# Performance work log

Hardware: AMD Instinct MI355X
Metric: run time of the kernel (lower is better)

The kernel has to match this reference:

```python
import jax, jax.numpy as jnp
import numpy as np

B, C, H, W, R = 8, 256, 64, 64, 16


def setup_inputs() -> dict:
    key = jax.random.key(0)
    ks = jax.random.split(key, 14)
    def w(k, shape, fan):
        return (jax.random.normal(k, shape, jnp.float32) / np.sqrt(fan)).astype(jnp.float32)
    return {
        "features_depth": jax.random.normal(ks[0], (B, C, H, W), jnp.float32),
        "features_semseg": jax.random.normal(ks[1], (B, C, H, W), jnp.float32),
        "W0": w(ks[2], (C, 2 * C), 2 * C),          # conv_split0 1x1, [out,in]
        "Wdw": w(ks[3], (C, 1, 3, 3), 9),            # depthwise 3x3, groups=C
        "Wq": w(ks[4], (C, C), C),                   # Linear weights [out,in]
        "Wk": w(ks[5], (C, C), C),
        "Wv": w(ks[6], (C, C), C),
        "Wp": w(ks[7], (C, C), C),
        "bp": jnp.zeros((C,), jnp.float32),
        "Wsplit": w(ks[8], (C, C), C),               # conv_split 1x1
        "se_d_w1": w(ks[9], (C // R, C), C),         # SE squeeze conv1x1 (depth)
        "se_d_w2": w(ks[10], (C, C // R), C // R),
        "se_s_w1": w(ks[11], (C // R, C), C),        # SE squeeze conv1x1 (semseg)
        "se_s_w2": w(ks[12], (C, C // R), C // R),
    }


def _l2norm(a, eps=1e-12):
    n = jnp.linalg.norm(a, axis=-1, keepdims=True)
    return a / jnp.maximum(n, eps)


def _se(x, w1, w2):
    # x: [B,C,H,W]; global avg pool -> 1x1 convs -> sigmoid gate
    p = x.mean(axis=(2, 3))                                  # [B,C]
    h = jax.nn.relu(jnp.einsum('rc,bc->br', w1, p))          # [B,C/R]
    g = jax.nn.sigmoid(jnp.einsum('cr,br->bc', w2, h))       # [B,C]
    return x * g[:, :, None, None]


def reference(features_depth, features_semseg, W0, Wdw, Wq, Wk, Wv, Wp, bp,
              Wsplit, se_d_w1, se_d_w2, se_s_w1, se_s_w2):
    x = jnp.concatenate([features_depth, features_semseg], axis=1)  # [B,2C,H,W]
    x = jnp.einsum('oc,bchw->bohw', W0, x)                          # 1x1 conv
    x = jax.lax.conv_general_dilated(
        x, Wdw, window_strides=(1, 1), padding='SAME',
        dimension_numbers=('NCHW', 'OIHW', 'NCHW'), feature_group_count=C)
    xt = x.transpose(0, 2, 3, 1).reshape(B, H * W, C)               # [B,N,C]
    q = (xt @ Wq.T).transpose(0, 2, 1)                              # [B,C,N]
    k = (xt @ Wk.T).transpose(0, 2, 1)
    v = (xt @ Wv.T).transpose(0, 2, 1)
    q = _l2norm(q)
    k = _l2norm(k)
    attn = jax.nn.softmax(jnp.einsum('bcn,bdn->bcd', k, q), axis=-1)  # [B,C,C]
    y = jnp.einsum('bcd,bdn->bcn', attn, v)                         # [B,C,N]
    y = y.transpose(0, 2, 1)                                        # [B,N,C]
    y = y @ Wp.T + bp                                               # proj
    out_c = y.reshape(B, H, W, C).transpose(0, 3, 1, 2)             # [B,C,H,W]
    out_c = jnp.einsum('oc,bchw->bohw', Wsplit, out_c)              # 1x1 conv
    out_depth = _se(out_c, se_d_w1, se_d_w2) + features_depth
    out_semseg = _se(out_c, se_s_w1, se_s_w2) + features_semseg
    return (out_depth, out_semseg)
```

## Files before the change

kernel.cpp:

```cpp
#include <hip/hip_runtime.h>
#include <cstdint>

#define DEVI __device__ __forceinline__

using fx4 = __attribute__((ext_vector_type(4))) float;
using bf8 = __attribute__((ext_vector_type(8))) __bf16;
using s8v = __attribute__((ext_vector_type(8))) short;
using s4v = __attribute__((ext_vector_type(4))) short;
typedef unsigned short u16;
typedef unsigned int u32;

DEVI float b2f(u16 u) { return __builtin_bit_cast(float, (u32)u << 16); }
DEVI u16 f2b(float f) {
  u32 u = __builtin_bit_cast(u32, f);
  return (u16)((u + 0x7fffu + ((u >> 16) & 1u)) >> 16);
}

#define GLOAD(g, l)                                                          \
  __builtin_amdgcn_global_load_lds(                                          \
      (const __attribute__((address_space(1))) unsigned int*)(g),            \
      (__attribute__((address_space(3))) unsigned int*)(l), 16, 0, 0)

__global__ __launch_bounds__(256) void prep(const float* __restrict__ W0,
                                            const float* __restrict__ Wq,
                                            const float* __restrict__ Wk,
                                            const float* __restrict__ Wv,
                                            u16* __restrict__ w0b,
                                            u16* __restrict__ wqk2,
                                            u16* __restrict__ wvtb) {
  const int i = blockIdx.x * 256 + threadIdx.x;
  if (blockIdx.y == 0) {
    if (i < 131072) w0b[i] = f2b(W0[i]);
  } else if (blockIdx.y == 1) {
    if (i < 524288) {
      const int row = i >> 9, c = i & 511;
      const float* src = (row < 256) ? Wq : Wk;
      wqk2[i] = f2b(src[((row & 255) << 8) + (c & 255)]);
    }
  } else {
    if (i < 65536) {
      const int e = i >> 8, d = i & 255;
      wvtb[i] = f2b(Wv[d * 256 + e]);
    }
  }
}

__global__ __launch_bounds__(256) void wcmul(const float* __restrict__ Wsp,
                                             const float* __restrict__ Wp,
                                             const float* __restrict__ bp,
                                             u16* __restrict__ wcb, float* __restrict__ bc) {
  const int o = blockIdx.x, t = threadIdx.x;
  __shared__ float row[256];
  __shared__ float red[4];
  row[t] = Wsp[o * 256 + t];
  __syncthreads();
  float acc = 0.f;
  for (int c = 0; c < 256; ++c) acc += row[c] * Wp[c * 256 + t];
  wcb[o * 256 + t] = f2b(acc);
  float pb = row[t] * bp[t];
#pragma unroll
  for (int m = 32; m > 0; m >>= 1) pb += __shfl_xor(pb, m);
  if ((t & 63) == 0) red[t >> 6] = pb;
  __syncthreads();
  if (t == 0) bc[o] = red[0] + red[1] + red[2] + red[3];
}

__global__ void pack_cat(const float* __restrict__ fd, const float* __restrict__ fs,
                         u16* __restrict__ out) {
  __shared__ float t[32][33];
  const int b = blockIdx.z;
  const int n0 = blockIdx.x * 32;
  const int g = blockIdx.y;
  const float* src = (g < 8) ? fd : fs;
  const int c0 = (g & 7) * 32;
  const int ccol0 = g * 32;
  const int tx = threadIdx.x;
  const int ty = threadIdx.y;
  const float* sp = src + ((long)b * 256 + c0) * 4096 + n0;
#pragma unroll
  for (int i = 0; i < 4; ++i) {
    int c = ty + i * 8;
    t[c][tx] = sp[(long)c * 4096 + tx];
  }
  __syncthreads();
  u16* op = out + ((long)b * 4096 + n0) * 512 + ccol0;
#pragma unroll
  for (int i = 0; i < 4; ++i) {
    int r = ty + i * 8;
    op[(long)r * 512 + tx] = f2b(t[tx][r]);
  }
}

template <typename OT, int BIAS, bool POOL>
__global__ __launch_bounds__(256) void gemm_nt(
    const u16* __restrict__ A, long sA, int lda,
    const u16* __restrict__ B, long sB, int ldb,
    OT* __restrict__ C, long sC, long sCs, int ldc,
    const float* __restrict__ bias, int Keff, int ksplit,
    float* __restrict__ poolpart) {
  __shared__ u16 ldsA[128 * 64];
  __shared__ u16 ldsB[128 * 64];
  const int z = blockIdx.z;
  const int bb = z / ksplit;
  const int ss = z - bb * ksplit;
  const int bm = blockIdx.x * 128;
  const int bn = blockIdx.y * 128;
  const u16* Ab = A + bb * sA + (long)ss * Keff + (long)bm * lda;
  const u16* Bb = B + bb * sB + (long)ss * Keff + (long)bn * ldb;
  const int tid = threadIdx.x;
  const int wid = tid >> 6;
  const int lane = tid & 63;
  const int wm = wid >> 1, wn = wid & 1;
  const int srow = tid >> 3;
  const int slot = tid & 7;

  fx4 acc[4][4] = {};
  for (int kt = 0; kt < Keff; kt += 64) {
#pragma unroll
    for (int i = 0; i < 4; ++i) {
      const int row = i * 32 + srow;
      const int kq = slot ^ (row & 7);
      GLOAD(Ab + (long)row * lda + kt + kq * 8, &ldsA[i * 2048 + wid * 512]);
      GLOAD(Bb + (long)row * ldb + kt + kq * 8, &ldsB[i * 2048 + wid * 512]);
    }
    __syncthreads();
#pragma unroll
    for (int ko = 0; ko < 2; ++ko) {
      bf8 af[4], bfr[4];
      const int kq = ko * 4 + (lane >> 4);
#pragma unroll
      for (int f = 0; f < 4; ++f) {
        const int ar = wm * 64 + f * 16 + (lane & 15);
        af[f] = *(const bf8*)&ldsA[ar * 64 + ((kq ^ (ar & 7)) * 8)];
        const int br = wn * 64 + f * 16 + (lane & 15);
        bfr[f] = *(const bf8*)&ldsB[br * 64 + ((kq ^ (br & 7)) * 8)];
      }
#pragma unroll
      for (int fm = 0; fm < 4; ++fm)
#pragma unroll
        for (int fn = 0; fn < 4; ++fn)
          acc[fm][fn] = __builtin_amdgcn_mfma_f32_16x16x32_bf16(af[fm], bfr[fn], acc[fm][fn], 0, 0, 0);
    }
    __syncthreads();
  }
  OT* Cb = C + bb * sC + ss * sCs;
  float pr[4][4];
  if (POOL) {
#pragma unroll
    for (int fm = 0; fm < 4; ++fm)
#pragma unroll
      for (int r = 0; r < 4; ++r) pr[fm][r] = 0.f;
  }
#pragma unroll
  for (int fm = 0; fm < 4; ++fm) {
    const int m0 = bm + wm * 64 + fm * 16 + ((lane >> 4) << 2);
#pragma unroll
    for (int fn = 0; fn < 4; ++fn) {
      const int n0 = bn + wn * 64 + fn * 16 + (lane & 15);
#pragma unroll
      for (int r = 0; r < 4; ++r) {
        float v = acc[fm][fn][r];
        if (BIAS == 2) v += bias[m0 + r];
        if constexpr (sizeof(OT) == 2) Cb[(long)(m0 + r) * ldc + n0] = (OT)f2b(v);
        else Cb[(long)(m0 + r) * ldc + n0] = v;
        if (POOL) pr[fm][r] += v;
      }
    }
  }
  if (POOL) {
#pragma unroll
    for (int fm = 0; fm < 4; ++fm)
#pragma unroll
      for (int r = 0; r < 4; ++r) {
        float s = pr[fm][r];
        s += __shfl_xor(s, 1); s += __shfl_xor(s, 2);
        s += __shfl_xor(s, 4); s += __shfl_xor(s, 8);
        if ((lane & 15) == 0) {
          const int o = bm + wm * 64 + fm * 16 + ((lane >> 4) << 2) + r;
          poolpart[(long)(blockIdx.y * 2 + wn) * 2048 + bb * 256 + o] = s;
        }
      }
  }
}

__global__ __launch_bounds__(256) void dwconv3x3(const u16* __restrict__ x,
                                                 const float* __restrict__ wdw,
                                                 u16* __restrict__ y) {
  __shared__ float w[9][256];
  const int t = threadIdx.x;
  for (int i = t; i < 2304; i += 256) w[i % 9][i / 9] = wdw[i];
  __syncthreads();
  const int nb = blockIdx.x;
  const int b = nb >> 9;
  const int n0 = (nb & 511) << 3;
  const int tn = t >> 5;
  const int tc = (t & 31) << 3;
  const int n = n0 + tn;
  const int hh = n >> 6, ww2 = n & 63;
  const u16* base = x + ((long)b << 20);
  float acc[8] = {0.f, 0.f, 0.f, 0.f, 0.f, 0.f, 0.f, 0.f};
#pragma unroll
  for (int ky = 0; ky < 3; ++ky) {
    const int hy = hh + ky - 1;
    if ((unsigned)hy >= 64u) continue;
#pragma unroll
    for (int kx = 0; kx < 3; ++kx) {
      const int wx = ww2 + kx - 1;
      if ((unsigned)wx >= 64u) continue;
      const s8v v = *(const s8v*)&base[(((hy << 6) + wx) << 8) + tc];
      const int kk = ky * 3 + kx;
      const fx4 wa = *(const fx4*)&w[kk][tc];
      const fx4 wb = *(const fx4*)&w[kk][tc + 4];
#pragma unroll
      for (int j = 0; j < 4; ++j) {
        acc[j] += wa[j] * b2f((u16)v[j]);
        acc[4 + j] += wb[j] * b2f((u16)v[4 + j]);
      }
    }
  }
  s8v o;
#pragma unroll
  for (int j = 0; j < 8; ++j) o[j] = (short)f2b(acc[j]);
  *(s8v*)&y[((long)b << 20) + ((long)n << 8) + tc] = o;
}

__global__ void btrans(const u16* __restrict__ x, u16* __restrict__ y) {
  __shared__ u16 t[32][34];
  const int b = blockIdx.z;
  const int n0 = blockIdx.x * 32;
  const int c0 = blockIdx.y * 32;
  const int tx = threadIdx.x, ty = threadIdx.y;
  const u16* sp = x + (long)b * 1048576 + (long)n0 * 256 + c0;
#pragma unroll
  for (int j = 0; j < 4; ++j) {
    int i = ty + j * 8;
    t[i][tx] = sp[(long)i * 256 + tx];
  }
  __syncthreads();
  u16* op = y + (long)b * 1048576 + (long)c0 * 4096 + n0;
#pragma unroll
  for (int j = 0; j < 4; ++j) {
    int r = ty + j * 8;
    op[(long)r * 4096 + tx] = t[tx][r];
  }
}

__global__ __launch_bounds__(256) void gsplit(const float* __restrict__ part,
                                              u16* __restrict__ G2) {
  const int i4 = (blockIdx.x * 256 + threadIdx.x) * 4;
  fx4 s = {0.f, 0.f, 0.f, 0.f};
#pragma unroll
  for (int ss = 0; ss < 8; ++ss) s += *(const fx4*)(part + (long)ss * 524288 + i4);
  const int b = i4 >> 16, rem = i4 & 65535, e = rem >> 8, c0 = rem & 255;
  u16* d = G2 + (long)b * 131072 + (long)e * 512 + c0;
  s4v hi, lo;
#pragma unroll
  for (int j = 0; j < 4; ++j) {
    u16 h = f2b(s[j]);
    hi[j] = (short)h;
    lo[j] = (short)f2b(s[j] - b2f(h));
  }
  *(s4v*)d = hi;
  *(s4v*)(d + 256) = lo;
}

__global__ __launch_bounds__(256) void ssplit_diag(const float* __restrict__ SS,
                                                   const float* __restrict__ Wq,
                                                   const float* __restrict__ Wk,
                                                   u16* __restrict__ S2,
                                                   float* __restrict__ rinv) {
  const int wid = threadIdx.x >> 6, lane = threadIdx.x & 63;
  const int gid = blockIdx.x * 4 + wid;
  const int b = gid >> 9, row = gid & 511;
  const float* ssrow = SS + (long)b * 131072 + (long)row * 256;
  const float* wrow = (row < 256) ? (Wq + row * 256) : (Wk + (row - 256) * 256);
  const fx4 sv = ((const fx4*)ssrow)[lane];
  const fx4 wv = ((const fx4*)wrow)[lane];
  float dot = sv[0] * wv[0] + sv[1] * wv[1] + sv[2] * wv[2] + sv[3] * wv[3];
#pragma unroll
  for (int o = 32; o > 0; o >>= 1) dot += __shfl_xor(dot, o);
  if (lane == 0)
    rinv[b * 512 + row] = 1.f / fmaxf(sqrtf(fmaxf(dot, 0.f)), 1e-12f);
  if (row < 256) {
    u16* d = S2 + (long)b * 131072 + (long)row * 512 + lane * 4;
    s4v hi, lo;
#pragma unroll
    for (int j = 0; j < 4; ++j) {
      u16 h = f2b(sv[j]);
      hi[j] = (short)h;
      lo[j] = (short)f2b(sv[j] - b2f(h));
    }
    *(s4v*)d = hi;
    *(s4v*)(d + 256) = lo;
  }
}

__global__ __launch_bounds__(256) void softmax_g(const float* __restrict__ araw,
                                                 const float* __restrict__ rinv,
                                                 u16* __restrict__ out) {
  const int wid = threadIdx.x >> 6, lane = threadIdx.x & 63;
  const long row = (long)blockIdx.x * 4 + wid;
  const int b = (int)(row >> 8);
  const int c = (int)(row & 255);
  fx4 v = ((const fx4*)(araw + row * 256))[lane];
  const float rk = rinv[b * 512 + 256 + c];
  const fx4 rq = *(const fx4*)&rinv[b * 512 + lane * 4];
  v[0] *= rk * rq[0]; v[1] *= rk * rq[1]; v[2] *= rk * rq[2]; v[3] *= rk * rq[3];
  float m = fmaxf(fmaxf(v[0], v[1]), fmaxf(v[2], v[3]));
#pragma unroll
  for (int o = 32; o > 0; o >>= 1) m = fmaxf(m, __shfl_xor(m, o));
  float e0 = __expf(v[0] - m), e1 = __expf(v[1] - m);
  float e2 = __expf(v[2] - m), e3 = __expf(v[3] - m);
  float s4 = e0 + e1 + e2 + e3;
#pragma unroll
  for (int o = 32; o > 0; o >>= 1) s4 += __shfl_xor(s4, o);
  const float inv = 1.f / s4;
  u16* op = out + row * 256 + lane * 4;
  op[0] = f2b(e0 * inv); op[1] = f2b(e1 * inv);
  op[2] = f2b(e2 * inv); op[3] = f2b(e3 * inv);
}

__global__ __launch_bounds__(256) void se_gates(const float* __restrict__ poolpart,
                                                const float* __restrict__ w1d, const float* __restrict__ w2d,
                                                const float* __restrict__ w1s, const float* __restrict__ w2s,
                                                float* __restrict__ gd, float* __restrict__ gs) {
  const int b = blockIdx.x;
  const int t = threadIdx.x;
  __shared__ float p[256], hd[16], hs[16];
  float s = 0.f;
#pragma unroll 8
  for (int sl = 0; sl < 64; ++sl) s += poolpart[(long)sl * 2048 + b * 256 + t];
  p[t] = s * (1.f / 4096.f);
  __syncthreads();
  if (t < 16) {
    float ad = 0.f, as2 = 0.f;
    for (int j = 0; j < 256; ++j) {
      ad += w1d[t * 256 + j] * p[j];
      as2 += w1s[t * 256 + j] * p[j];
    }
    hd[t] = fmaxf(ad, 0.f);
    hs[t] = fmaxf(as2, 0.f);
  }
  __syncthreads();
  float ad = 0.f, as2 = 0.f;
#pragma unroll
  for (int r = 0; r < 16; ++r) {
    ad += w2d[t * 16 + r] * hd[r];
    as2 += w2s[t * 16 + r] * hs[r];
  }
  gd[b * 256 + t] = 1.f / (1.f + __expf(-ad));
  gs[b * 256 + t] = 1.f / (1.f + __expf(-as2));
}

__global__ __launch_bounds__(256) void fuse_out(const u16* __restrict__ oc,
                                                const float* __restrict__ gd, const float* __restrict__ gs,
                                                const float* __restrict__ fd, const float* __restrict__ fs,
                                                float* __restrict__ od, float* __restrict__ os) {
  const long i = ((long)blockIdx.x * 256 + threadIdx.x) * 8;
  const long bc = i >> 12;
  const float gdv = gd[bc], gsv = gs[bc];
  const s8v c8 = *(const s8v*)&oc[i];
  const fx4 a0 = *(const fx4*)(fd + i), a1 = *(const fx4*)(fd + i + 4);
  const fx4 s0 = *(const fx4*)(fs + i), s1 = *(const fx4*)(fs + i + 4);
  fx4 d0, d1, e0, e1;
#pragma unroll
  for (int j = 0; j < 4; ++j) {
    const float cl = b2f((u16)c8[j]);
    const float ch = b2f((u16)c8[4 + j]);
    d0[j] = cl * gdv + a0[j]; d1[j] = ch * gdv + a1[j];
    e0[j] = cl * gsv + s0[j]; e1[j] = ch * gsv + s1[j];
  }
  *(fx4*)(od + i) = d0; *(fx4*)(od + i + 4) = d1;
  *(fx4*)(os + i) = e0; *(fx4*)(os + i + 4) = e1;
}

extern "C" void kernel_launch(void* const* d_in, const int* in_sizes, int n_in,
                              void* d_out, int out_size, void* d_ws, size_t ws_size,
                              hipStream_t stream) {
  const float* fd  = (const float*)d_in[0];
  const float* fs  = (const float*)d_in[1];
  const float* W0  = (const float*)d_in[2];
  const float* Wdw = (const float*)d_in[3];
  const float* Wq  = (const float*)d_in[4];
  const float* Wk  = (const float*)d_in[5];
  const float* Wv  = (const float*)d_in[6];
  const float* Wp  = (const float*)d_in[7];
  const float* bp  = (const float*)d_in[8];
  const float* Wsp = (const float*)d_in[9];
  const float* w1d = (const float*)d_in[10];
  const float* w2d = (const float*)d_in[11];
  const float* w1s = (const float*)d_in[12];
  const float* w2s = (const float*)d_in[13];

  char* ws = (char*)d_ws;
  u16* catb   = (u16*)(ws + 0);
  u16* xtT    = (u16*)(ws + 0);
  u16* x0b    = (u16*)(ws + 33554432);
  u16* outcb  = x0b;
  u16* xtb    = (u16*)(ws + 50331648);
  float* part = (float*)(ws + 67108864);
  u16* G2     = (u16*)(ws + 83886080);
  float* SS   = (float*)(ws + 85983232);
  u16* S2     = (u16*)(ws + 90177536);
  float* araw = (float*)(ws + 92274688);
  u16* attnb  = (u16*)(ws + 94371840);
  u16* m1t    = (u16*)(ws + 95420416);
  u16* wfin   = (u16*)(ws + 96468992);
  u16* w0b    = (u16*)(ws + 97517568);
  u16* wqk2   = (u16*)(ws + 97779712);
  u16* wvtb   = (u16*)(ws + 98304000);
  u16* wcb    = (u16*)(ws + 98435072);
  float* bcb  = (float*)(ws + 98566144);
  float* rinv = (float*)(ws + 98567168);
  float* poolpart = (float*)(ws + 98583552);
  float* gdp  = (float*)(ws + 99108864);
  float* gsp  = (float*)(ws + 99117056);
  float* od  = (float*)d_out;
  float* osg = od + 8388608;

  prep<<<dim3(2048, 3), 256, 0, stream>>>(W0, Wq, Wk, Wv, w0b, wqk2, wvtb);
  wcmul<<<256, 256, 0, stream>>>(Wsp, Wp, bp, wcb, bcb);
  pack_cat<<<dim3(128, 16, 8), dim3(32, 8), 0, stream>>>(fd, fs, catb);
  gemm_nt<u16, 0, false><<<dim3(32, 2, 8), 256, 0, stream>>>(
      catb, 2097152, 512, w0b, 0, 512, x0b, 1048576, 0, 256, nullptr, 512, 1, nullptr);
  dwconv3x3<<<4096, 256, 0, stream>>>(x0b, Wdw, xtb);
  btrans<<<dim3(128, 8, 8), dim3(32, 8), 0, stream>>>(xtb, xtT);
  gemm_nt<float, 0, false><<<dim3(2, 2, 64), 256, 0, stream>>>(
      xtT, 1048576, 4096, xtT, 1048576, 4096,
      part, 65536, 524288, 256, nullptr, 512, 8, nullptr);
  gsplit<<<512, 256, 0, stream>>>(part, G2);
  gemm_nt<float, 0, false><<<dim3(4, 2, 8), 256, 0, stream>>>(
      wqk2, 0, 512, G2, 131072, 512, SS, 131072, 0, 256, nullptr, 512, 1, nullptr);
  ssplit_diag<<<1024, 256, 0, stream>>>(SS, Wq, Wk, S2, rinv);
  gemm_nt<float, 0, false><<<dim3(2, 2, 8), 256, 0, stream>>>(
      wqk2 + 131072, 0, 512, S2, 131072, 512, araw, 65536, 0, 256, nullptr, 512, 1, nullptr);
  softmax_g<<<512, 256, 0, stream>>>(araw, rinv, attnb);
  gemm_nt<u16, 0, false><<<dim3(2, 2, 8), 256, 0, stream>>>(
      wvtb, 0, 256, attnb, 65536, 256, m1t, 65536, 0, 256, nullptr, 256, 1, nullptr);
  gemm_nt<u16, 0, false><<<dim3(2, 2, 8), 256, 0, stream>>>(
      wcb, 0, 256, m1t, 65536, 256, wfin, 65536, 0, 256, nullptr, 256, 1, nullptr);
  gemm_nt<u16, 2, true><<<dim3(2, 32, 8), 256, 0, stream>>>(
      wfin, 65536, 256, xtb, 1048576, 256, outcb, 1048576, 0, 4096, bcb, 256, 1, poolpart);
  se_gates<<<8, 256, 0, stream>>>(poolpart, w1d, w2d, w1s, w2s, gdp, gsp);
  fuse_out<<<4096, 256, 0, stream>>>(outcb, gdp, gsp, fd, fs, od, osg);
}
```

Baseline: 183.9 us.

## Fuse dwconv with transpose, fold ssplit into GEMM epilogue, residual from bf16 cat

The depthwise conv now also writes the channel-major transposed copy through LDS, which removes the separate btrans kernel. The Gram GEMM uses a deeper K per split with fewer splits, so gsplit sums 4 partials instead of 8. The SS GEMM epilogue writes the hi/lo bf16 split directly and computes the partial diagonal norms, which removes ssplit_diag and its fp32 SS buffer. Softmax now reduces those partials itself. The final fuse reads the residual from the bf16 packed concat instead of the fp32 inputs, which cuts traffic but rounds the residual add to bf16 precision.

```diff
diff --git a/kernel.cpp b/kernel.cpp
--- a/kernel.cpp
+++ b/kernel.cpp
@@ -91,13 +91,15 @@
   }
 }
 
-template <typename OT, int BIAS, bool POOL>
+template <typename OT, int BIAS, bool POOL, int EPI>
 __global__ __launch_bounds__(256) void gemm_nt(
     const u16* __restrict__ A, long sA, int lda,
     const u16* __restrict__ B, long sB, int ldb,
     OT* __restrict__ C, long sC, long sCs, int ldc,
     const float* __restrict__ bias, int Keff, int ksplit,
-    float* __restrict__ poolpart) {
+    float* __restrict__ poolpart,
+    const float* __restrict__ wqf, const float* __restrict__ wkf,
+    float* __restrict__ dpart) {
   __shared__ u16 ldsA[128 * 64];
   __shared__ u16 ldsB[128 * 64];
   const int z = blockIdx.z;
@@ -143,6 +145,47 @@
     }
     __syncthreads();
   }
+  if constexpr (EPI == 1) {
+    u16* S2b = (u16*)C + bb * sC;
+    float dp[4][4];
+#pragma unroll
+    for (int fm = 0; fm < 4; ++fm)
+#pragma unroll
+      for (int r = 0; r < 4; ++r) dp[fm][r] = 0.f;
+#pragma unroll
+    for (int fm = 0; fm < 4; ++fm) {
+      const int m0 = bm + wm * 64 + fm * 16 + ((lane >> 4) << 2);
+#pragma unroll
+      for (int fn = 0; fn < 4; ++fn) {
+        const int n0 = bn + wn * 64 + fn * 16 + (lane & 15);
+#pragma unroll
+        for (int r = 0; r < 4; ++r) {
+          const float v = acc[fm][fn][r];
+          const int m = m0 + r;
+          if (m < 256) {
+            const u16 hi = f2b(v);
+            S2b[(long)m * 512 + n0] = hi;
+            S2b[(long)m * 512 + 256 + n0] = f2b(v - b2f(hi));
+          }
+          const float* wr = (m < 256) ? (wqf + (long)m * 256) : (wkf + (long)(m - 256) * 256);
+          dp[fm][r] += v * wr[n0];
+        }
+      }
+    }
+#pragma unroll
+    for (int fm = 0; fm < 4; ++fm)
+#pragma unroll
+      for (int r = 0; r < 4; ++r) {
+        float s = dp[fm][r];
+        s += __shfl_xor(s, 1); s += __shfl_xor(s, 2);
+        s += __shfl_xor(s, 4); s += __shfl_xor(s, 8);
+        if ((lane & 15) == 0) {
+          const int m = bm + wm * 64 + fm * 16 + ((lane >> 4) << 2) + r;
+          dpart[(long)(blockIdx.y * 2 + wn) * 4096 + bb * 512 + m] = s;
+        }
+      }
+    return;
+  }
   OT* Cb = C + bb * sC + ss * sCs;
   float pr[4][4];
   if (POOL) {
@@ -183,66 +226,53 @@
   }
 }
 
-__global__ __launch_bounds__(256) void dwconv3x3(const u16* __restrict__ x,
-                                                 const float* __restrict__ wdw,
-                                                 u16* __restrict__ y) {
-  __shared__ float w[9][256];
+__global__ __launch_bounds__(256) void dwconv2(const u16* __restrict__ x,
+                                               const float* __restrict__ wdw,
+                                               u16* __restrict__ y,
+                                               u16* __restrict__ yT) {
+  __shared__ float wsm[9][256];
+  __shared__ u16 tb[256][72];
   const int t = threadIdx.x;
-  for (int i = t; i < 2304; i += 256) w[i % 9][i / 9] = wdw[i];
-  __syncthreads();
-  const int nb = blockIdx.x;
-  const int b = nb >> 9;
-  const int n0 = (nb & 511) << 3;
-  const int tn = t >> 5;
-  const int tc = (t & 31) << 3;
-  const int n = n0 + tn;
-  const int hh = n >> 6, ww2 = n & 63;
+  for (int i = t; i < 2304; i += 256) wsm[i % 9][i / 9] = wdw[i];
+  const int b = blockIdx.x >> 6, h = blockIdx.x & 63;
+  const int c8 = (t & 31) * 8, wsub = t >> 5;
   const u16* base = x + ((long)b << 20);
-  float acc[8] = {0.f, 0.f, 0.f, 0.f, 0.f, 0.f, 0.f, 0.f};
-#pragma unroll
-  for (int ky = 0; ky < 3; ++ky) {
-    const int hy = hh + ky - 1;
-    if ((unsigned)hy >= 64u) continue;
-#pragma unroll
-    for (int kx = 0; kx < 3; ++kx) {
-      const int wx = ww2 + kx - 1;
-      if ((unsigned)wx >= 64u) continue;
-      const s8v v = *(const s8v*)&base[(((hy << 6) + wx) << 8) + tc];
-      const int kk = ky * 3 + kx;
-      const fx4 wa = *(const fx4*)&w[kk][tc];
-      const fx4 wb = *(const fx4*)&w[kk][tc + 4];
-#pragma unroll
-      for (int j = 0; j < 4; ++j) {
-        acc[j] += wa[j] * b2f((u16)v[j]);
-        acc[4 + j] += wb[j] * b2f((u16)v[4 + j]);
-      }
-    }
-  }
-  s8v o;
-#pragma unroll
-  for (int j = 0; j < 8; ++j) o[j] = (short)f2b(acc[j]);
-  *(s8v*)&y[((long)b << 20) + ((long)n << 8) + tc] = o;
-}
-
-__global__ void btrans(const u16* __restrict__ x, u16* __restrict__ y) {
-  __shared__ u16 t[32][34];
-  const int b = blockIdx.z;
-  const int n0 = blockIdx.x * 32;
-  const int c0 = blockIdx.y * 32;
-  const int tx = threadIdx.x, ty = threadIdx.y;
-  const u16* sp = x + (long)b * 1048576 + (long)n0 * 256 + c0;
-#pragma unroll
-  for (int j = 0; j < 4; ++j) {
-    int i = ty + j * 8;
-    t[i][tx] = sp[(long)i * 256 + tx];
-  }
-  __syncthreads();
-  u16* op = y + (long)b * 1048576 + (long)c0 * 4096 + n0;
-#pragma unroll
-  for (int j = 0; j < 4; ++j) {
-    int r = ty + j * 8;
-    op[(long)r * 4096 + tx] = t[tx][r];
-  }
+  __syncthreads();
+#pragma unroll
+  for (int i = 0; i < 8; ++i) {
+    const int w = wsub + 8 * i;
+    float acc[8] = {0.f, 0.f, 0.f, 0.f, 0.f, 0.f, 0.f, 0.f};
+#pragma unroll
+    for (int ky = 0; ky < 3; ++ky) {
+      const int hy = h + ky - 1;
+      if ((unsigned)hy >= 64u) continue;
+#pragma unroll
+      for (int kx = 0; kx < 3; ++kx) {
+        const int wx = w + kx - 1;
+        if ((unsigned)wx >= 64u) continue;
+        const s8v v = *(const s8v*)&base[(((hy << 6) + wx) << 8) + c8];
+        const int kk = ky * 3 + kx;
+        const fx4 wa = *(const fx4*)&wsm[kk][c8];
+        const fx4 wb = *(const fx4*)&wsm[kk][c8 + 4];
+#pragma unroll
+        for (int j = 0; j < 4; ++j) {
+          acc[j] += wa[j] * b2f((u16)v[j]);
+          acc[4 + j] += wb[j] * b2f((u16)v[4 + j]);
+        }
+      }
+    }
+    s8v o;
+#pragma unroll
+    for (int j = 0; j < 8; ++j) o[j] = (short)f2b(acc[j]);
+    *(s8v*)&y[((long)b << 20) + (long)(((h << 6) + w) << 8) + c8] = o;
+#pragma unroll
+    for (int j = 0; j < 8; ++j) tb[c8 + j][w] = (u16)o[j];
+  }
+  __syncthreads();
+  u16* dst = yT + ((long)b << 20) + (long)t * 4096 + (h << 6);
+#pragma unroll
+  for (int j = 0; j < 8; ++j)
+    *(s8v*)&dst[j * 8] = *(const s8v*)&tb[t][j * 8];
 }
 
 __global__ __launch_bounds__(256) void gsplit(const float* __restrict__ part,
@@ -250,7 +280,7 @@
   const int i4 = (blockIdx.x * 256 + threadIdx.x) * 4;
   fx4 s = {0.f, 0.f, 0.f, 0.f};
 #pragma unroll
-  for (int ss = 0; ss < 8; ++ss) s += *(const fx4*)(part + (long)ss * 524288 + i4);
+  for (int ss = 0; ss < 4; ++ss) s += *(const fx4*)(part + (long)ss * 524288 + i4);
   const int b = i4 >> 16, rem = i4 & 65535, e = rem >> 8, c0 = rem & 255;
   u16* d = G2 + (long)b * 131072 + (long)e * 512 + c0;
   s4v hi, lo;
@@ -264,48 +294,25 @@
   *(s4v*)(d + 256) = lo;
 }
 
-__global__ __launch_bounds__(256) void ssplit_diag(const float* __restrict__ SS,
-                                                   const float* __restrict__ Wq,
-                                                   const float* __restrict__ Wk,
-                                                   u16* __restrict__ S2,
-                                                   float* __restrict__ rinv) {
+__global__ __launch_bounds__(256) void softmax_g2(const float* __restrict__ araw,
+                                                  const float* __restrict__ dpart,
+                                                  u16* __restrict__ out) {
   const int wid = threadIdx.x >> 6, lane = threadIdx.x & 63;
-  const int gid = blockIdx.x * 4 + wid;
-  const int b = gid >> 9, row = gid & 511;
-  const float* ssrow = SS + (long)b * 131072 + (long)row * 256;
-  const float* wrow = (row < 256) ? (Wq + row * 256) : (Wk + (row - 256) * 256);
-  const fx4 sv = ((const fx4*)ssrow)[lane];
-  const fx4 wv = ((const fx4*)wrow)[lane];
-  float dot = sv[0] * wv[0] + sv[1] * wv[1] + sv[2] * wv[2] + sv[3] * wv[3];
-#pragma unroll
-  for (int o = 32; o > 0; o >>= 1) dot += __shfl_xor(dot, o);
-  if (lane == 0)
-    rinv[b * 512 + row] = 1.f / fmaxf(sqrtf(fmaxf(dot, 0.f)), 1e-12f);
-  if (row < 256) {
-    u16* d = S2 + (long)b * 131072 + (long)row * 512 + lane * 4;
-    s4v hi, lo;
-#pragma unroll
-    for (int j = 0; j < 4; ++j) {
-      u16 h = f2b(sv[j]);
-      hi[j] = (short)h;
-      lo[j] = (short)f2b(sv[j] - b2f(h));
-    }
-    *(s4v*)d = hi;
-    *(s4v*)(d + 256) = lo;
-  }
-}
-
-__global__ __launch_bounds__(256) void softmax_g(const float* __restrict__ araw,
-                                                 const float* __restrict__ rinv,
-                                                 u16* __restrict__ out) {
-  const int wid = threadIdx.x >> 6, lane = threadIdx.x & 63;
+  const int t = threadIdx.x;
+  const int b = blockIdx.x >> 6;
+  __shared__ float rq[256];
+  float dq = dpart[b * 512 + t] + dpart[4096 + b * 512 + t] +
+             dpart[8192 + b * 512 + t] + dpart[12288 + b * 512 + t];
+  rq[t] = 1.f / fmaxf(sqrtf(fmaxf(dq, 0.f)), 1e-12f);
+  __syncthreads();
   const long row = (long)blockIdx.x * 4 + wid;
-  const int b = (int)(row >> 8);
   const int c = (int)(row & 255);
+  const int ki = b * 512 + 256 + c;
+  float dk = dpart[ki] + dpart[4096 + ki] + dpart[8192 + ki] + dpart[12288 + ki];
+  const float rk = 1.f / fmaxf(sqrtf(fmaxf(dk, 0.f)), 1e-12f);
   fx4 v = ((const fx4*)(araw + row * 256))[lane];
-  const float rk = rinv[b * 512 + 256 + c];
-  const fx4 rq = *(const fx4*)&rinv[b * 512 + lane * 4];
-  v[0] *= rk * rq[0]; v[1] *= rk * rq[1]; v[2] *= rk * rq[2]; v[3] *= rk * rq[3];
+  v[0] *= rk * rq[lane * 4];     v[1] *= rk * rq[lane * 4 + 1];
+  v[2] *= rk * rq[lane * 4 + 2]; v[3] *= rk * rq[lane * 4 + 3];
   float m = fmaxf(fmaxf(v[0], v[1]), fmaxf(v[2], v[3]));
 #pragma unroll
   for (int o = 32; o > 0; o >>= 1) m = fmaxf(m, __shfl_xor(m, o));
@@ -352,26 +359,47 @@
   gs[b * 256 + t] = 1.f / (1.f + __expf(-as2));
 }
 
-__global__ __launch_bounds__(256) void fuse_out(const u16* __restrict__ oc,
-                                                const float* __restrict__ gd, const float* __restrict__ gs,
-                                                const float* __restrict__ fd, const float* __restrict__ fs,
-                                                float* __restrict__ od, float* __restrict__ os) {
-  const long i = ((long)blockIdx.x * 256 + threadIdx.x) * 8;
-  const long bc = i >> 12;
-  const float gdv = gd[bc], gsv = gs[bc];
-  const s8v c8 = *(const s8v*)&oc[i];
-  const fx4 a0 = *(const fx4*)(fd + i), a1 = *(const fx4*)(fd + i + 4);
-  const fx4 s0 = *(const fx4*)(fs + i), s1 = *(const fx4*)(fs + i + 4);
-  fx4 d0, d1, e0, e1;
+__global__ __launch_bounds__(256) void fuse_out2(const u16* __restrict__ oc,
+                                                 const u16* __restrict__ cat,
+                                                 const float* __restrict__ gd,
+                                                 const float* __restrict__ gs,
+                                                 float* __restrict__ od,
+                                                 float* __restrict__ os) {
+  __shared__ u16 td[32][68];
+  __shared__ u16 ts2[32][68];
+  const int b = blockIdx.z;
+  const int c0 = blockIdx.y * 32;
+  const int n0 = blockIdx.x * 64;
+  const int t = threadIdx.x;
+  {
+    const int n = t >> 2, cj = (t & 3) * 8;
+    const u16* cb = cat + ((long)b * 4096 + n0 + n) * 512 + c0 + cj;
+    const s8v vd = *(const s8v*)cb;
+    const s8v vs = *(const s8v*)(cb + 256);
+#pragma unroll
+    for (int j = 0; j < 8; ++j) {
+      td[cj + j][n] = (u16)vd[j];
+      ts2[cj + j][n] = (u16)vs[j];
+    }
+  }
+  __syncthreads();
+  const int c = t >> 3, no = (t & 7) * 8;
+  const long obase = ((long)b * 256 + c0 + c) * 4096 + n0 + no;
+  const float gdv = gd[b * 256 + c0 + c];
+  const float gsv = gs[b * 256 + c0 + c];
+  const s8v o8 = *(const s8v*)&oc[obase];
+  fx4 r0, r1, q0, q1;
 #pragma unroll
   for (int j = 0; j < 4; ++j) {
-    const float cl = b2f((u16)c8[j]);
-    const float ch = b2f((u16)c8[4 + j]);
-    d0[j] = cl * gdv + a0[j]; d1[j] = ch * gdv + a1[j];
-    e0[j] = cl * gsv + s0[j]; e1[j] = ch * gsv + s1[j];
-  }
-  *(fx4*)(od + i) = d0; *(fx4*)(od + i + 4) = d1;
-  *(fx4*)(os + i) = e0; *(fx4*)(os + i + 4) = e1;
+    const float vl = b2f((u16)o8[j]);
+    const float vh = b2f((u16)o8[4 + j]);
+    r0[j] = vl * gdv + b2f(td[c][no + j]);
+    r1[j] = vh * gdv + b2f(td[c][no + 4 + j]);
+    q0[j] = vl * gsv + b2f(ts2[c][no + j]);
+    q1[j] = vh * gsv + b2f(ts2[c][no + 4 + j]);
+  }
+  *(fx4*)(od + obase) = r0; *(fx4*)(od + obase + 4) = r1;
+  *(fx4*)(os + obase) = q0; *(fx4*)(os + obase + 4) = q1;
 }
 
 extern "C" void kernel_launch(void* const* d_in, const int* in_sizes, int n_in,
@@ -394,53 +422,56 @@
 
   char* ws = (char*)d_ws;
   u16* catb   = (u16*)(ws + 0);
-  u16* xtT    = (u16*)(ws + 0);
   u16* x0b    = (u16*)(ws + 33554432);
   u16* outcb  = x0b;
   u16* xtb    = (u16*)(ws + 50331648);
-  float* part = (float*)(ws + 67108864);
-  u16* G2     = (u16*)(ws + 83886080);
-  float* SS   = (float*)(ws + 85983232);
-  u16* S2     = (u16*)(ws + 90177536);
-  float* araw = (float*)(ws + 92274688);
-  u16* attnb  = (u16*)(ws + 94371840);
-  u16* m1t    = (u16*)(ws + 95420416);
-  u16* wfin   = (u16*)(ws + 96468992);
-  u16* w0b    = (u16*)(ws + 97517568);
-  u16* wqk2   = (u16*)(ws + 97779712);
-  u16* wvtb   = (u16*)(ws + 98304000);
-  u16* wcb    = (u16*)(ws + 98435072);
-  float* bcb  = (float*)(ws + 98566144);
-  float* rinv = (float*)(ws + 98567168);
-  float* poolpart = (float*)(ws + 98583552);
-  float* gdp  = (float*)(ws + 99108864);
-  float* gsp  = (float*)(ws + 99117056);
+  u16* xtT    = (u16*)(ws + 67108864);
+  float* part = (float*)(ws + 83886080);
+  u16* G2     = (u16*)(ws + 92274688);
+  u16* S2     = (u16*)(ws + 94371840);
+  float* araw = (float*)(ws + 96468992);
+  u16* attnb  = (u16*)(ws + 98566144);
+  u16* m1t    = (u16*)(ws + 99614720);
+  u16* wfin   = (u16*)(ws + 100663296);
+  u16* w0b    = (u16*)(ws + 101711872);
+  u16* wqk2   = (u16*)(ws + 101974016);
+  u16* wvtb   = (u16*)(ws + 102498304);
+  u16* wcb    = (u16*)(ws + 102629376);
+  float* bcb  = (float*)(ws + 102760448);
+  float* dpart = (float*)(ws + 102761472);
+  float* poolpart = (float*)(ws + 102827008);
+  float* gdp  = (float*)(ws + 103351296);
+  float* gsp  = (float*)(ws + 103359488);
   float* od  = (float*)d_out;
   float* osg = od + 8388608;
 
   prep<<<dim3(2048, 3), 256, 0, stream>>>(W0, Wq, Wk, Wv, w0b, wqk2, wvtb);
   wcmul<<<256, 256, 0, stream>>>(Wsp, Wp, bp, wcb, bcb);
   pack_cat<<<dim3(128, 16, 8), dim3(32, 8), 0, stream>>>(fd, fs, catb);
-  gemm_nt<u16, 0, false><<<dim3(32, 2, 8), 256, 0, stream>>>(
-      catb, 2097152, 512, w0b, 0, 512, x0b, 1048576, 0, 256, nullptr, 512, 1, nullptr);
-  dwconv3x3<<<4096, 256, 0, stream>>>(x0b, Wdw, xtb);
-  btrans<<<dim3(128, 8, 8), dim3(32, 8), 0, stream>>>(xtb, xtT);
-  gemm_nt<float, 0, false><<<dim3(2, 2, 64), 256, 0, stream>>>(
+  gemm_nt<u16, 0, false, 0><<<dim3(32, 2, 8), 256, 0, stream>>>(
+      catb, 2097152, 512, w0b, 0, 512, x0b, 1048576, 0, 256, nullptr, 512, 1,
+      nullptr, nullptr, nullptr, nullptr);
+  dwconv2<<<512, 256, 0, stream>>>(x0b, Wdw, xtb, xtT);
+  gemm_nt<float, 0, false, 0><<<dim3(2, 2, 32), 256, 0, stream>>>(
       xtT, 1048576, 4096, xtT, 1048576, 4096,
-      part, 65536, 524288, 256, nullptr, 512, 8, nullptr);
+      part, 65536, 524288, 256, nullptr, 1024, 4, nullptr, nullptr, nullptr, nullptr);
   gsplit<<<512, 256, 0, stream>>>(part, G2);
-  gemm_nt<float, 0, false><<<dim3(4, 2, 8), 256, 0, stream>>>(
-      wqk2, 0, 512, G2, 131072, 512, SS, 131072, 0, 256, nullptr, 512, 1, nullptr);
-  ssplit_diag<<<1024, 256, 0, stream>>>(SS, Wq, Wk, S2, rinv);
-  gemm_nt<float, 0, false><<<dim3(2, 2, 8), 256, 0, stream>>>(
-      wqk2 + 131072, 0, 512, S2, 131072, 512, araw, 65536, 0, 256, nullptr, 512, 1, nullptr);
-  softmax_g<<<512, 256, 0, stream>>>(araw, rinv, attnb);
-  gemm_nt<u16, 0, false><<<dim3(2, 2, 8), 256, 0, stream>>>(
-      wvtb, 0, 256, attnb, 65536, 256, m1t, 65536, 0, 256, nullptr, 256, 1, nullptr);
-  gemm_nt<u16, 0, false><<<dim3(2, 2, 8), 256, 0, stream>>>(
-      wcb, 0, 256, m1t, 65536, 256, wfin, 65536, 0, 256, nullptr, 256, 1, nullptr);
-  gemm_nt<u16, 2, true><<<dim3(2, 32, 8), 256, 0, stream>>>(
-      wfin, 65536, 256, xtb, 1048576, 256, outcb, 1048576, 0, 4096, bcb, 256, 1, poolpart);
+  gemm_nt<u16, 0, false, 1><<<dim3(4, 2, 8), 256, 0, stream>>>(
+      wqk2, 0, 512, G2, 131072, 512, S2, 131072, 0, 512, nullptr, 512, 1,
+      nullptr, Wq, Wk, dpart);
+  gemm_nt<float, 0, false, 0><<<dim3(2, 2, 8), 256, 0, stream>>>(
+      wqk2 + 131072, 0, 512, S2, 131072, 512, araw, 65536, 0, 256, nullptr, 512, 1,
+      nullptr, nullptr, nullptr, nullptr);
+  softmax_g2<<<512, 256, 0, stream>>>(araw, dpart, attnb);
+  gemm_nt<u16, 0, false, 0><<<dim3(2, 2, 8), 256, 0, stream>>>(
+      wvtb, 0, 256, attnb, 65536, 256, m1t, 65536, 0, 256, nullptr, 256, 1,
+      nullptr, nullptr, nullptr, nullptr);
+  gemm_nt<u16, 0, false, 0><<<dim3(2, 2, 8), 256, 0, stream>>>(
+      wcb, 0, 256, m1t, 65536, 256, wfin, 65536, 0, 256, nullptr, 256, 1,
+      nullptr, nullptr, nullptr, nullptr);
+  gemm_nt<u16, 2, true, 0><<<dim3(2, 32, 8), 256, 0, stream>>>(
+      wfin, 65536, 256, xtb, 1048576, 256, outcb, 1048576, 0, 4096, bcb, 256, 1,
+      poolpart, nullptr, nullptr, nullptr);
   se_gates<<<8, 256, 0, stream>>>(poolpart, w1d, w2d, w1s, w2s, gdp, gsp);
-  fuse_out<<<4096, 256, 0, stream>>>(outcb, gdp, gsp, fd, fs, od, osg);
-}
+  fuse_out2<<<dim3(64, 8, 8), 256, 0, stream>>>(outcb, catb, gdp, gsp, od, osg);
+}
```

New measurement: 198.4 us. +7.9%, slower.
